# Kernel tuning notes

Hardware: AMD Instinct MI355X
Metric: run time of the kernel (lower is better)

## Reference

```python
import jax, jax.numpy as jnp
import numpy as np

N = 131072        # total points
NUM_SEG = 128     # number of point clouds / segments
INC = 3
HID = 128
OUTC = 128
NUM_LAYER = 6
NUM_INNER = 2
EPS = 1e-3        # ACN eps
CLAMP_MIN = 1e-3  # clamp(min=0.001) on normalizer


def setup_inputs() -> dict:
    key = jax.random.key(0)
    ks = jax.random.split(key, 10)
    s = 0.05
    x = jax.random.normal(ks[0], (N, INC), dtype=jnp.float32)
    segment_idx = jnp.sort(jax.random.randint(ks[1], (N,), 0, NUM_SEG, dtype=jnp.int32))
    weight_pri = jax.random.uniform(ks[2], (N,), dtype=jnp.float32)
    Win0 = jax.random.normal(ks[3], (INC, HID), dtype=jnp.float32) * s
    bin0 = jnp.zeros((HID,), jnp.float32)
    Win_rest = jax.random.normal(ks[4], (4, HID, HID), dtype=jnp.float32) * s
    bin_rest = jnp.zeros((4, HID), jnp.float32)
    # 6 ResBlocks x 2 inner ConvLayers: Linear(128,128) + ACN(att Linear(128,1)) + relu
    conv_W = jax.random.normal(ks[5], (NUM_LAYER, NUM_INNER, HID, HID), dtype=jnp.float32) * s
    conv_b = jnp.zeros((NUM_LAYER, NUM_INNER, HID), jnp.float32)
    att_W = jax.random.normal(ks[6], (NUM_LAYER, NUM_INNER, HID, 1), dtype=jnp.float32) * s
    att_b = jnp.zeros((NUM_LAYER, NUM_INNER, 1), jnp.float32)
    # output Mlp: Linear(128,128)+lrelu, Linear(128,128)
    out_W = jax.random.normal(ks[7], (2, HID, OUTC), dtype=jnp.float32) * s
    out_b = jnp.zeros((2, OUTC), jnp.float32)
    return dict(x=x, segment_idx=segment_idx, weight_pri=weight_pri,
                Win0=Win0, bin0=bin0, Win_rest=Win_rest, bin_rest=bin_rest,
                conv_W=conv_W, conv_b=conv_b, att_W=att_W, att_b=att_b,
                out_W=out_W, out_b=out_b)


def _seg_sum(v, seg):
    return jax.ops.segment_sum(v, seg, num_segments=NUM_SEG)


def _scatter_softmax(att, seg):
    # stable softmax within segments; att: [N, 1]
    m = jax.ops.segment_max(att, seg, num_segments=NUM_SEG)
    e = jnp.exp(att - m[seg])
    return e / _seg_sum(e, seg)[seg]


def _acn(x, aw, ab, seg, wp):
    # attentive context normalization; x: [N, HID]
    a = _scatter_softmax(x @ aw + ab, seg)          # [N, 1]
    a = a * wp[:, None]
    a = a / jnp.clip(_seg_sum(a, seg)[seg], CLAMP_MIN)
    mean = _seg_sum(x * a, seg)[seg]
    out = x - mean
    std = jnp.sqrt(_seg_sum(a * out * out, seg)[seg] + EPS)
    return out / std, a


def reference(x, segment_idx, weight_pri, Win0, bin0, Win_rest, bin_rest,
              conv_W, conv_b, att_W, att_b, out_W, out_b):
    lrelu = jax.nn.leaky_relu  # slope 0.01, matches nn.LeakyReLU default
    # input Mlp + outer leaky_relu in Acne.forward
    h = lrelu(x @ Win0 + bin0)
    for i in range(3):
        h = lrelu(h @ Win_rest[i] + bin_rest[i])
    h = h @ Win_rest[3] + bin_rest[3]
    h = lrelu(h)
    last_a = None
    for li in range(NUM_LAYER):
        xin = h
        for j in range(NUM_INNER):
            xin = xin @ conv_W[li, j] + conv_b[li, j]
            xin, last_a = _acn(xin, att_W[li, j], att_b[li, j], segment_idx, weight_pri)
            xin = jax.nn.relu(xin)
        h = xin + h  # residual
    h = lrelu(h @ out_W[0] + out_b[0])
    h = h @ out_W[1] + out_b[1]
    return h, last_a
```

## Files before the change

### kernel.cpp

```cpp
#include <hip/hip_runtime.h>

#define N_PTS 131072
#define NSEG 128
#define SW 132

typedef unsigned short u16;
typedef __attribute__((ext_vector_type(8))) short short8;
typedef __attribute__((ext_vector_type(8))) unsigned short ushort8;
typedef __attribute__((ext_vector_type(4))) float f32x4;

__device__ __forceinline__ float b2f(u16 u){union{unsigned v;float f;}x;x.v=((unsigned)u)<<16;return x.f;}
__device__ __forceinline__ u16 f2b(float f){unsigned u=__float_as_uint(f);u+=0x7FFFu+((u>>16)&1u);return (u16)(u>>16);}

__global__ __launch_bounds__(256) void k_zero(float* __restrict__ M0, float* __restrict__ Q0,
                                              float* __restrict__ Z0, float* __restrict__ W0){
  int t = blockIdx.x * 256 + threadIdx.x;
  M0[t] = 0.f; Q0[t] = 0.f;
  if (t < 128) { Z0[t] = 0.f; W0[t] = 0.f; }
}

__global__ __launch_bounds__(256) void k_wpack(const float* __restrict__ Wr,
    const float* __restrict__ convW, const float* __restrict__ outW,
    const float* __restrict__ attW, const float* __restrict__ attb,
    const float* __restrict__ convb,
    u16* __restrict__ Wf, float* __restrict__ uAtt, float* __restrict__ cAtt){
  int mat = blockIdx.x;
  const float* W = (mat<4) ? (Wr+mat*16384) : (mat<16) ? (convW+(mat-4)*16384) : (outW+(mat-16)*16384);
  u16* dst = Wf + mat*16384;
  for (int t = threadIdx.x; t < 16384; t += 256){ int n=t>>7,k=t&127; dst[t]=f2b(W[k*128+n]); }
  if (mat>=4 && mat<16){
    int l = mat-4;
    __syncthreads();
    int tid = threadIdx.x;
    if (tid < 128){
      float s = 0.f;
      for (int c=0;c<128;c++) s += b2f(dst[c*128+tid]) * attW[l*128+c];
      uAtt[l*128+tid] = s;
    } else if (tid == 128){
      float s = attb[l];
      for (int c=0;c<128;c++) s += convb[l*128+c] * attW[l*128+c];
      cAtt[l] = s;
    }
  }
}

__global__ __launch_bounds__(256) void k_in0(const float* __restrict__ x,
    const float* __restrict__ W0, const float* __restrict__ b0, u16* __restrict__ Tb){
  int gid = blockIdx.x*256 + threadIdx.x;
  int n = gid>>7, c = gid&127;
  float acc = b0[c] + x[n*3]*W0[c] + x[n*3+1]*W0[128+c] + x[n*3+2]*W0[256+c];
  Tb[gid] = f2b(acc > 0.f ? acc : 0.01f*acc);
}

template<bool WH>
__global__ __launch_bounds__(256) void k_mlp(u16* __restrict__ Tb, float* __restrict__ A0,
    const u16* __restrict__ Wfm, const float* __restrict__ Bv){
  __shared__ u16 Xs[128*SW];
  const int tid=threadIdx.x, wave=tid>>6, lane=tid&63, q=lane>>4, m16=lane&15;
  const int row0=blockIdx.x*128;
  const u16* Xb = Tb + (size_t)row0*128;
  #pragma unroll
  for (int i=0;i<8;i++){
    int e8=i*2048+tid*8; int rloc=e8>>7, c8=e8&127;
    *(ushort8*)&Xs[rloc*SW+c8] = *(const ushort8*)&Xb[rloc*128+c8];
  }
  short8 bfr[2][4];
  #pragma unroll
  for (int ct=0;ct<2;ct++){
    int n = wave*32 + 2*m16 + ct;
    #pragma unroll
    for (int kc=0;kc<4;kc++) bfr[ct][kc] = *(const short8*)&Wfm[n*128+kc*32+q*8];
  }
  const int cA = wave*32 + 2*m16;
  const float bias0=Bv[cA], bias1=Bv[cA+1];
  __syncthreads();
  #pragma unroll
  for (int rt=0;rt<8;rt++){
    int r0=rt*16;
    short8 af[4];
    #pragma unroll
    for (int kc=0;kc<4;kc++) af[kc] = *(const short8*)&Xs[(r0+m16)*SW+kc*32+q*8];
    f32x4 a0={0,0,0,0}, a1={0,0,0,0};
    #pragma unroll
    for (int kc=0;kc<4;kc++){
      a0=__builtin_amdgcn_mfma_f32_16x16x32_bf16(af[kc],bfr[0][kc],a0,0,0,0);
      a1=__builtin_amdgcn_mfma_f32_16x16x32_bf16(af[kc],bfr[1][kc],a1,0,0,0);
    }
    #pragma unroll
    for (int t=0;t<4;t++){
      int rloc=r0+q*4+t;
      float v0=a0[t]+bias0, v1=a1[t]+bias1;
      v0=v0>0.f?v0:0.01f*v0; v1=v1>0.f?v1:0.01f*v1;
      size_t wi=(size_t)(row0+rloc)*64 + wave*16 + m16;
      ((unsigned*)Tb)[wi] = (unsigned)f2b(v0) | ((unsigned)f2b(v1)<<16);
      if (WH) { float2 h={v0,v1}; ((float2*)A0)[wi]=h; }
    }
  }
}

template<int IN>
__global__ __launch_bounds__(256) void k_conv(u16* __restrict__ Tb, float* __restrict__ A0,
    const u16* __restrict__ Wfm, const float* __restrict__ Bv,
    const float* __restrict__ uL, const float* __restrict__ cL,
    float* __restrict__ L, const int* __restrict__ seg, const float* __restrict__ wp,
    const float* __restrict__ pZ, const float* __restrict__ pW,
    const float* __restrict__ pM, const float* __restrict__ pQ,
    float* __restrict__ cZ, float* __restrict__ cW,
    float* __restrict__ cM, float* __restrict__ cQ,
    float* __restrict__ nZ, float* __restrict__ nW,
    float* __restrict__ nM, float* __restrict__ nQ){
  __shared__ u16 Xs[128*SW];
  __shared__ float rowP[128];
  __shared__ float eS[128], aS[128];
  __shared__ int sgS[128];
  const int tid=threadIdx.x, wave=tid>>6, lane=tid&63, q=lane>>4, m16=lane&15;
  const int row0=blockIdx.x*128;

  if (tid<16){ nM[blockIdx.x*16+tid]=0.f; nQ[blockIdx.x*16+tid]=0.f; }
  if (blockIdx.x==0 && tid<128){ nZ[tid]=0.f; nW[tid]=0.f; }

  const int c8 = (tid*8)&127;
  float uv[8];
  { float4 u0=*(const float4*)&uL[c8]; float4 u1=*(const float4*)&uL[c8+4];
    uv[0]=u0.x;uv[1]=u0.y;uv[2]=u0.z;uv[3]=u0.w;uv[4]=u1.x;uv[5]=u1.y;uv[6]=u1.z;uv[7]=u1.w; }

  const u16* Xb = Tb + (size_t)row0*128;
  #pragma unroll
  for (int i=0;i<8;i++){
    int rloc = i*16 + (tid>>4);
    ushort8 raw = *(const ushort8*)&Xb[rloc*128+c8];
    float v[8];
    if (IN==1){
      #pragma unroll
      for (int j=0;j<8;j++) v[j]=b2f(raw[j]);
      *(ushort8*)&Xs[rloc*SW+c8] = raw;
    } else {
      int gr=row0+rloc, s=seg[gr];
      float Z=pZ[s], Wd=pW[s];
      float invd = 1.f/fmaxf(Wd, fmaxf(1e-3f*Z, 1e-30f));
      float sa = Wd*invd;
      float4 mn0=*(const float4*)&pM[s*128+c8];
      float4 mn1=*(const float4*)&pM[s*128+c8+4];
      float4 q0=*(const float4*)&pQ[s*128+c8];
      float4 q1=*(const float4*)&pQ[s*128+c8+4];
      float mn[8]={mn0.x,mn0.y,mn0.z,mn0.w,mn1.x,mn1.y,mn1.z,mn1.w};
      float qv[8]={q0.x,q0.y,q0.z,q0.w,q1.x,q1.y,q1.z,q1.w};
      #pragma unroll
      for (int j=0;j<8;j++){
        float m=mn[j]*invd, m2=qv[j]*invd;
        v[j]=fmaxf((b2f(raw[j])-m)*rsqrtf(m2+(sa-2.f)*m*m+1e-3f),0.f);
      }
      if (IN==3){
        float4 h0=*(const float4*)&A0[(size_t)gr*128+c8];
        float4 h1=*(const float4*)&A0[(size_t)gr*128+c8+4];
        v[0]+=h0.x;v[1]+=h0.y;v[2]+=h0.z;v[3]+=h0.w;
        v[4]+=h1.x;v[5]+=h1.y;v[6]+=h1.z;v[7]+=h1.w;
        float4 w0={v[0],v[1],v[2],v[3]}, w1={v[4],v[5],v[6],v[7]};
        *(float4*)&A0[(size_t)gr*128+c8]=w0;
        *(float4*)&A0[(size_t)gr*128+c8+4]=w1;
      }
      ushort8 ob;
      #pragma unroll
      for (int j=0;j<8;j++) ob[j]=f2b(v[j]);
      *(ushort8*)&Xs[rloc*SW+c8]=ob;
    }
    float p = v[0]*uv[0]+v[1]*uv[1]+v[2]*uv[2]+v[3]*uv[3]
            + v[4]*uv[4]+v[5]*uv[5]+v[6]*uv[6]+v[7]*uv[7];
    p += __shfl_xor(p,1,64); p += __shfl_xor(p,2,64);
    p += __shfl_xor(p,4,64); p += __shfl_xor(p,8,64);
    if (m16==0) rowP[rloc]=p;
  }

  short8 bfr[2][4];
  #pragma unroll
  for (int ct=0;ct<2;ct++){
    int n = wave*32 + 2*m16 + ct;
    #pragma unroll
    for (int kc=0;kc<4;kc++) bfr[ct][kc]=*(const short8*)&Wfm[n*128+kc*32+q*8];
  }
  const int cA = wave*32 + 2*m16;
  const float bias0=Bv[cA], bias1=Bv[cA+1];
  __syncthreads();

  if (tid<128){
    int r=row0+tid;
    float l=rowP[tid]+cL[0];
    float e=__expf(fminf(l,60.f));
    float sw=e*wp[r];
    L[r]=sw;
    eS[tid]=e; aS[tid]=sw; sgS[tid]=seg[r];
  }
  __syncthreads();
  if (tid<128){
    int s=sgS[tid];
    if (tid==0 || sgS[tid-1]!=s){
      float se=0.f, ss=0.f;
      for (int i=tid;i<128 && sgS[i]==s;i++){ se+=eS[i]; ss+=aS[i]; }
      atomicAdd(&cZ[s],se); atomicAdd(&cW[s],ss);
    }
  }

  const int s0=sgS[0], s127=sgS[127];
  const bool uni = (s0==s127);
  int cur = uni ? s0 : sgS[q*4];
  float sx0=0.f,sq0=0.f,sx1=0.f,sq1=0.f;

  #pragma unroll
  for (int rt=0;rt<8;rt++){
    int r0=rt*16;
    short8 af[4];
    #pragma unroll
    for (int kc=0;kc<4;kc++) af[kc]=*(const short8*)&Xs[(r0+m16)*SW+kc*32+q*8];
    f32x4 a0={0,0,0,0}, a1={0,0,0,0};
    #pragma unroll
    for (int kc=0;kc<4;kc++){
      a0=__builtin_amdgcn_mfma_f32_16x16x32_bf16(af[kc],bfr[0][kc],a0,0,0,0);
      a1=__builtin_amdgcn_mfma_f32_16x16x32_bf16(af[kc],bfr[1][kc],a1,0,0,0);
    }
    #pragma unroll
    for (int t=0;t<4;t++){
      int rloc=r0+q*4+t;
      float v0=a0[t]+bias0, v1=a1[t]+bias1;
      ((unsigned*)Tb)[(size_t)(row0+rloc)*64 + wave*16 + m16] =
          (unsigned)f2b(v0) | ((unsigned)f2b(v1)<<16);
      float a = aS[rloc];
      if (!uni){
        int s = sgS[rloc];
        if (s != cur){
          atomicAdd(&cM[cur*128+cA],sx0);  atomicAdd(&cQ[cur*128+cA],sq0);
          atomicAdd(&cM[cur*128+cA+1],sx1);atomicAdd(&cQ[cur*128+cA+1],sq1);
          sx0=sq0=sx1=sq1=0.f; cur=s;
        }
      }
      sx0 += a*v0; sq0 += a*v0*v0;
      sx1 += a*v1; sq1 += a*v1*v1;
    }
  }
  if (uni){
    sx0 += __shfl_xor(sx0,16,64); sx0 += __shfl_xor(sx0,32,64);
    sq0 += __shfl_xor(sq0,16,64); sq0 += __shfl_xor(sq0,32,64);
    sx1 += __shfl_xor(sx1,16,64); sx1 += __shfl_xor(sx1,32,64);
    sq1 += __shfl_xor(sq1,16,64); sq1 += __shfl_xor(sq1,32,64);
    if (q==0){
      atomicAdd(&cM[s0*128+cA],sx0);  atomicAdd(&cQ[s0*128+cA],sq0);
      atomicAdd(&cM[s0*128+cA+1],sx1);atomicAdd(&cQ[s0*128+cA+1],sq1);
    }
  } else {
    atomicAdd(&cM[cur*128+cA],sx0);  atomicAdd(&cQ[cur*128+cA],sq0);
    atomicAdd(&cM[cur*128+cA+1],sx1);atomicAdd(&cQ[cur*128+cA+1],sq1);
  }
}

__global__ __launch_bounds__(256) void k_megaout(const u16* __restrict__ Tb,
    const float* __restrict__ A0, const u16* __restrict__ Wf16, const float* __restrict__ outb,
    const int* __restrict__ seg, const float* __restrict__ L,
    const float* __restrict__ pZ, const float* __restrict__ pW,
    const float* __restrict__ pM, const float* __restrict__ pQ,
    float* __restrict__ Of, float* __restrict__ a_out){
  __shared__ u16 buf[2*128*SW];
  const int tid=threadIdx.x, wave=tid>>6, lane=tid&63, q=lane>>4, m16=lane&15;
  const int row0=blockIdx.x*128;
  const u16* Xb = Tb + (size_t)row0*128;
  #pragma unroll
  for (int i=0;i<8;i++){
    int e8=i*2048+tid*8; int rloc=e8>>7, c8=e8&127;
    ushort8 raw=*(const ushort8*)&Xb[rloc*128+c8];
    int gr=row0+rloc, s=seg[gr];
    float Z=pZ[s], Wd=pW[s];
    float invd=1.f/fmaxf(Wd, fmaxf(1e-3f*Z,1e-30f));
    float sa=Wd*invd;
    float4 mn0=*(const float4*)&pM[s*128+c8];
    float4 mn1=*(const float4*)&pM[s*128+c8+4];
    float4 q0=*(const float4*)&pQ[s*128+c8];
    float4 q1=*(const float4*)&pQ[s*128+c8+4];
    float mn[8]={mn0.x,mn0.y,mn0.z,mn0.w,mn1.x,mn1.y,mn1.z,mn1.w};
    float qv[8]={q0.x,q0.y,q0.z,q0.w,q1.x,q1.y,q1.z,q1.w};
    float4 h0=*(const float4*)&A0[(size_t)gr*128+c8];
    float4 h1=*(const float4*)&A0[(size_t)gr*128+c8+4];
    float hv[8]={h0.x,h0.y,h0.z,h0.w,h1.x,h1.y,h1.z,h1.w};
    ushort8 ob;
    #pragma unroll
    for (int j=0;j<8;j++){
      float m=mn[j]*invd, m2=qv[j]*invd;
      ob[j]=f2b(fmaxf((b2f(raw[j])-m)*rsqrtf(m2+(sa-2.f)*m*m+1e-3f),0.f)+hv[j]);
    }
    *(ushort8*)&buf[rloc*SW+c8]=ob;
  }
  if (tid<128){
    int r=row0+tid, s=seg[r];
    float invd=1.f/fmaxf(pW[s], fmaxf(1e-3f*pZ[s],1e-30f));
    a_out[r]=L[r]*invd;
  }
  __syncthreads();
  const int cA=wave*32+2*m16;
  {
    u16* dst=buf+128*SW;
    short8 bfr[2][4];
    #pragma unroll
    for (int ct=0;ct<2;ct++){
      int n=wave*32+2*m16+ct;
      #pragma unroll
      for (int kc=0;kc<4;kc++) bfr[ct][kc]=*(const short8*)&Wf16[n*128+kc*32+q*8];
    }
    float bias0=outb[cA], bias1=outb[cA+1];
    #pragma unroll
    for (int rt=0;rt<8;rt++){
      int r0=rt*16;
      short8 af[4];
      #pragma unroll
      for (int kc=0;kc<4;kc++) af[kc]=*(const short8*)&buf[(r0+m16)*SW+kc*32+q*8];
      f32x4 a0={0,0,0,0}, a1={0,0,0,0};
      #pragma unroll
      for (int kc=0;kc<4;kc++){
        a0=__builtin_amdgcn_mfma_f32_16x16x32_bf16(af[kc],bfr[0][kc],a0,0,0,0);
        a1=__builtin_amdgcn_mfma_f32_16x16x32_bf16(af[kc],bfr[1][kc],a1,0,0,0);
      }
      #pragma unroll
      for (int t=0;t<4;t++){
        int rloc=r0+q*4+t;
        float v0=a0[t]+bias0, v1=a1[t]+bias1;
        v0=v0>0.f?v0:0.01f*v0; v1=v1>0.f?v1:0.01f*v1;
        dst[rloc*SW+cA]=f2b(v0);
        dst[rloc*SW+cA+1]=f2b(v1);
      }
    }
  }
  __syncthreads();
  {
    const u16* src=buf+128*SW;
    short8 bfr[2][4];
    #pragma unroll
    for (int ct=0;ct<2;ct++){
      int n=wave*32+2*m16+ct;
      #pragma unroll
      for (int kc=0;kc<4;kc++) bfr[ct][kc]=*(const short8*)&Wf16[16384+n*128+kc*32+q*8];
    }
    float bias0=outb[128+cA], bias1=outb[128+cA+1];
    #pragma unroll
    for (int rt=0;rt<8;rt++){
      int r0=rt*16;
      short8 af[4];
      #pragma unroll
      for (int kc=0;kc<4;kc++) af[kc]=*(const short8*)&src[(r0+m16)*SW+kc*32+q*8];
      f32x4 a0={0,0,0,0}, a1={0,0,0,0};
      #pragma unroll
      for (int kc=0;kc<4;kc++){
        a0=__builtin_amdgcn_mfma_f32_16x16x32_bf16(af[kc],bfr[0][kc],a0,0,0,0);
        a1=__builtin_amdgcn_mfma_f32_16x16x32_bf16(af[kc],bfr[1][kc],a1,0,0,0);
      }
      #pragma unroll
      for (int t=0;t<4;t++){
        int rloc=r0+q*4+t;
        float2 o={a0[t]+bias0, a1[t]+bias1};
        ((float2*)Of)[(size_t)(row0+rloc)*64 + wave*16 + m16]=o;
      }
    }
  }
}

extern "C" void kernel_launch(void* const* d_in, const int* in_sizes, int n_in,
                              void* d_out, int out_size, void* d_ws, size_t ws_size,
                              hipStream_t stream){
  const float* x     = (const float*)d_in[0];
  const int*   seg   = (const int*)d_in[1];
  const float* wp    = (const float*)d_in[2];
  const float* Win0  = (const float*)d_in[3];
  const float* bin0  = (const float*)d_in[4];
  const float* Wr    = (const float*)d_in[5];
  const float* br    = (const float*)d_in[6];
  const float* convW = (const float*)d_in[7];
  const float* convb = (const float*)d_in[8];
  const float* attW  = (const float*)d_in[9];
  const float* attb  = (const float*)d_in[10];
  const float* outW  = (const float*)d_in[11];
  const float* outb  = (const float*)d_in[12];

  float* A0 = (float*)d_ws;
  u16*   Tb = (u16*)(A0 + (size_t)N_PTS*128);
  float* L  = (float*)(Tb + (size_t)N_PTS*128);
  float* base = L + N_PTS;
  float* SZ[3], *SWt[3], *SM[3], *SQ[3];
  for (int p=0;p<3;p++){
    SZ[p]  = base + p*(128+128+16384+16384);
    SWt[p] = SZ[p] + 128;
    SM[p]  = SWt[p] + 128;
    SQ[p]  = SM[p] + 16384;
  }
  float* uAtt = base + 3*(128+128+16384+16384);
  float* cAtt = uAtt + 12*128;
  u16*   Wf   = (u16*)(cAtt + 16);

  float* Of    = (float*)d_out;
  float* a_out = (float*)d_out + (size_t)N_PTS*128;

  const int GB = N_PTS/128;

  k_zero<<<64,256,0,stream>>>(SM[0],SQ[0],SZ[0],SWt[0]);
  k_wpack<<<18,256,0,stream>>>(Wr, convW, outW, attW, attb, convb, Wf, uAtt, cAtt);
  k_in0<<<N_PTS*128/256,256,0,stream>>>(x, Win0, bin0, Tb);

  for (int i=0;i<3;i++)
    k_mlp<false><<<GB,256,0,stream>>>(Tb, nullptr, Wf+i*16384, br+i*128);
  k_mlp<true><<<GB,256,0,stream>>>(Tb, A0, Wf+3*16384, br+3*128);

  for (int j=0;j<12;j++){
    int wp_ = j%3, rp = (j+2)%3, np = (j+1)%3;
    const u16* Wm = Wf + (size_t)(4+j)*16384;
    const float* uj = uAtt + j*128;
    const float* cj = cAtt + j;
    if (j==0)
      k_conv<1><<<GB,256,0,stream>>>(Tb, nullptr, Wm, convb, uj, cj, L, seg, wp,
          nullptr,nullptr,nullptr,nullptr,
          SZ[wp_],SWt[wp_],SM[wp_],SQ[wp_], SZ[np],SWt[np],SM[np],SQ[np]);
    else if (j&1)
      k_conv<2><<<GB,256,0,stream>>>(Tb, nullptr, Wm, convb+j*128, uj, cj, L, seg, wp,
          SZ[rp],SWt[rp],SM[rp],SQ[rp],
          SZ[wp_],SWt[wp_],SM[wp_],SQ[wp_], SZ[np],SWt[np],SM[np],SQ[np]);
    else
      k_conv<3><<<GB,256,0,stream>>>(Tb, A0, Wm, convb+j*128, uj, cj, L, seg, wp,
          SZ[rp],SWt[rp],SM[rp],SQ[rp],
          SZ[wp_],SWt[wp_],SM[wp_],SQ[wp_], SZ[np],SWt[np],SM[np],SQ[np]);
  }

  k_megaout<<<GB,256,0,stream>>>(Tb, A0, Wf+(size_t)16*16384, outb, seg, L,
                                 SZ[2],SWt[2],SM[2],SQ[2], Of, a_out);
}
```

Before: 731.5 us.

## Fuse whole network into one cooperative persistent kernel with grid syncs

Replaces the chain of per-layer kernels (input MLP, 12 conv/ACN layers, output MLP) with a single cooperative kernel. Each block keeps its 128-row tile in LDS and the residual in registers across all layers, and uses grid.sync between layers to publish the segment statistics. This removes the global round trips of activations and the per-launch overhead. The cost is 1024 blocks that must all be co-resident (4 per CU), heavy register pressure from a 64-float residual array, and 12 grid-wide barriers. A fallback to the old multi-kernel path remains if occupancy is insufficient.

```diff
diff --git a/kernel.cpp b/kernel.cpp
--- a/kernel.cpp
+++ b/kernel.cpp
@@ -1,8 +1,12 @@
 #include <hip/hip_runtime.h>
+#include <hip/hip_cooperative_groups.h>
+
+namespace cg = cooperative_groups;
 
 #define N_PTS 131072
 #define NSEG 128
 #define SW 132
+#define PSTRIDE 33024
 
 typedef unsigned short u16;
 typedef __attribute__((ext_vector_type(8))) short short8;
@@ -11,13 +15,8 @@
 
 __device__ __forceinline__ float b2f(u16 u){union{unsigned v;float f;}x;x.v=((unsigned)u)<<16;return x.f;}
 __device__ __forceinline__ u16 f2b(float f){unsigned u=__float_as_uint(f);u+=0x7FFFu+((u>>16)&1u);return (u16)(u>>16);}
-
-__global__ __launch_bounds__(256) void k_zero(float* __restrict__ M0, float* __restrict__ Q0,
-                                              float* __restrict__ Z0, float* __restrict__ W0){
-  int t = blockIdx.x * 256 + threadIdx.x;
-  M0[t] = 0.f; Q0[t] = 0.f;
-  if (t < 128) { Z0[t] = 0.f; W0[t] = 0.f; }
-}
+__device__ __forceinline__ float aload(const float* p){ return __hip_atomic_load(p, __ATOMIC_RELAXED, __HIP_MEMORY_SCOPE_AGENT); }
+__device__ __forceinline__ void astore(float* p, float v){ __hip_atomic_store(p, v, __ATOMIC_RELAXED, __HIP_MEMORY_SCOPE_AGENT); }
 
 __global__ __launch_bounds__(256) void k_wpack(const float* __restrict__ Wr,
     const float* __restrict__ convW, const float* __restrict__ outW,
@@ -44,6 +43,311 @@
   }
 }
 
+__device__ __forceinline__ void gemm_lrelu_inplace(u16* Xs, const u16* __restrict__ Wm,
+    const float* __restrict__ Bv, int wave, int q, int m16){
+  short8 bfr[2][4];
+  const int cA = wave*32 + 2*m16;
+  #pragma unroll
+  for (int ct=0; ct<2; ct++){
+    int n = cA + ct;
+    #pragma unroll
+    for (int kc=0; kc<4; kc++) bfr[ct][kc] = *(const short8*)&Wm[n*128 + kc*32 + q*8];
+  }
+  const float b0 = Bv[cA], b1 = Bv[cA+1];
+  #pragma unroll
+  for (int rt=0; rt<8; rt++){
+    const int r0 = rt*16;
+    f32x4 a0={0,0,0,0}, a1={0,0,0,0};
+    short8 afn = *(const short8*)&Xs[(r0+m16)*SW + q*8];
+    #pragma unroll
+    for (int kc=0; kc<4; kc++){
+      short8 afc = afn;
+      if (kc<3) afn = *(const short8*)&Xs[(r0+m16)*SW + (kc+1)*32 + q*8];
+      a0 = __builtin_amdgcn_mfma_f32_16x16x32_bf16(afc, bfr[0][kc], a0, 0,0,0);
+      a1 = __builtin_amdgcn_mfma_f32_16x16x32_bf16(afc, bfr[1][kc], a1, 0,0,0);
+    }
+    __syncthreads();
+    #pragma unroll
+    for (int t=0; t<4; t++){
+      int rloc = r0 + q*4 + t;
+      float v0 = a0[t]+b0, v1 = a1[t]+b1;
+      v0 = v0>0.f ? v0 : 0.01f*v0;
+      v1 = v1>0.f ? v1 : 0.01f*v1;
+      *(unsigned*)&Xs[rloc*SW + cA] = (unsigned)f2b(v0) | ((unsigned)f2b(v1)<<16);
+    }
+  }
+}
+
+__global__ __launch_bounds__(256, 4) void k_fused(
+    const float* __restrict__ x, const int* __restrict__ seg, const float* __restrict__ wp,
+    const float* __restrict__ Win0, const float* __restrict__ bin0,
+    const float* __restrict__ br, const float* __restrict__ convb, const float* __restrict__ outb,
+    const u16* __restrict__ Wf, const float* __restrict__ uAtt, const float* __restrict__ cAtt,
+    float* __restrict__ Pstat, float* __restrict__ Of, float* __restrict__ a_out)
+{
+  __shared__ u16 Xs[128*SW];
+  __shared__ float rowP[128];
+  __shared__ float eS[128], aS[128];
+  __shared__ int   sgS[128];
+  __shared__ float wpS[128];
+  __shared__ float MhL[2][128], ScL[2][128];
+
+  const int tid=threadIdx.x, wave=tid>>6, lane=tid&63, q=lane>>4, m16=lane&15;
+  const int row0=blockIdx.x*128;
+  const int c8=(tid*8)&127;
+  const int rbase=tid>>4;
+
+  cg::grid_group grid = cg::this_grid();
+
+  if (tid<128){ sgS[tid]=seg[row0+tid]; wpS[tid]=wp[row0+tid]; }
+  if (tid<33){ int idx=blockIdx.x*33+tid; if (idx<PSTRIDE) astore(Pstat+idx, 0.f); }
+  __syncthreads();
+
+  const int sA=sgS[0], sB=sgS[127];
+  const bool uni=(sA==sB);
+  unsigned slotm=0;
+  #pragma unroll
+  for (int i=0;i<8;i++) if (sgS[i*16+rbase]!=sA) slotm|=1u<<i;
+
+  {
+    float w0[8],w1[8],w2[8],bv[8];
+    *(float4*)&w0[0]=*(const float4*)&Win0[c8];     *(float4*)&w0[4]=*(const float4*)&Win0[c8+4];
+    *(float4*)&w1[0]=*(const float4*)&Win0[128+c8]; *(float4*)&w1[4]=*(const float4*)&Win0[128+c8+4];
+    *(float4*)&w2[0]=*(const float4*)&Win0[256+c8]; *(float4*)&w2[4]=*(const float4*)&Win0[256+c8+4];
+    *(float4*)&bv[0]=*(const float4*)&bin0[c8];     *(float4*)&bv[4]=*(const float4*)&bin0[c8+4];
+    #pragma unroll
+    for (int i=0;i<8;i++){
+      int rloc=i*16+rbase, r=row0+rloc;
+      float x0=x[r*3], x1=x[r*3+1], x2=x[r*3+2];
+      ushort8 ob;
+      #pragma unroll
+      for (int jj=0;jj<8;jj++){
+        float v=bv[jj]+x0*w0[jj]+x1*w1[jj]+x2*w2[jj];
+        v=v>0.f?v:0.01f*v;
+        ob[jj]=f2b(v);
+      }
+      *(ushort8*)&Xs[rloc*SW+c8]=ob;
+    }
+  }
+  __syncthreads();
+
+  #pragma unroll 1
+  for (int l=0;l<4;l++){
+    gemm_lrelu_inplace(Xs, Wf + (size_t)l*16384, br + l*128, wave,q,m16);
+    __syncthreads();
+  }
+
+  grid.sync();
+
+  float h[64];
+
+  #pragma unroll 1
+  for (int j=0;j<12;j++){
+    float* Pw = Pstat + (j%3)*PSTRIDE;
+    const float* Pr = Pstat + ((j+2)%3)*PSTRIDE;
+    float* Pn = Pstat + ((j+1)%3)*PSTRIDE;
+
+    if (j>0){
+      int half=tid>>7, ch=tid&127;
+      int s = half ? sB : sA;
+      float Z=aload(Pr+s), Wd=aload(Pr+128+s);
+      float invd=1.f/fmaxf(Wd, fmaxf(1e-3f*Z, 1e-30f));
+      float sa=Wd*invd;
+      float m =aload(Pr+256  + s*128+ch)*invd;
+      float qv=aload(Pr+16640+ s*128+ch)*invd;
+      MhL[half][ch]=m;
+      ScL[half][ch]=rsqrtf(qv+(sa-2.f)*m*m+1e-3f);
+    }
+    float uv[8];
+    { float4 u0=*(const float4*)&uAtt[j*128+c8]; float4 u1=*(const float4*)&uAtt[j*128+c8+4];
+      uv[0]=u0.x;uv[1]=u0.y;uv[2]=u0.z;uv[3]=u0.w;uv[4]=u1.x;uv[5]=u1.y;uv[6]=u1.z;uv[7]=u1.w; }
+    const float cL0 = cAtt[j];
+    __syncthreads();
+
+    #pragma unroll
+    for (int i=0;i<8;i++){
+      const int rloc=i*16+rbase;
+      ushort8 raw=*(const ushort8*)&Xs[rloc*SW+c8];
+      float v[8];
+      if (j==0){
+        #pragma unroll
+        for (int jj=0;jj<8;jj++){ v[jj]=b2f(raw[jj]); h[i*8+jj]=v[jj]; }
+      } else {
+        const int sl=(slotm>>i)&1;
+        #pragma unroll
+        for (int jj=0;jj<8;jj++){
+          float vv=(b2f(raw[jj])-MhL[sl][c8+jj])*ScL[sl][c8+jj];
+          vv=fmaxf(vv,0.f);
+          if ((j&1)==0){ vv+=h[i*8+jj]; h[i*8+jj]=vv; }
+          v[jj]=vv;
+        }
+        ushort8 ob;
+        #pragma unroll
+        for (int jj=0;jj<8;jj++) ob[jj]=f2b(v[jj]);
+        *(ushort8*)&Xs[rloc*SW+c8]=ob;
+      }
+      float p = v[0]*uv[0]+v[1]*uv[1]+v[2]*uv[2]+v[3]*uv[3]
+              + v[4]*uv[4]+v[5]*uv[5]+v[6]*uv[6]+v[7]*uv[7];
+      p += __shfl_xor(p,1,64); p += __shfl_xor(p,2,64);
+      p += __shfl_xor(p,4,64); p += __shfl_xor(p,8,64);
+      if (m16==0) rowP[rloc]=p;
+    }
+    __syncthreads();
+
+    if (tid<128){
+      float l2=rowP[tid]+cL0;
+      float e=__expf(fminf(l2,60.f));
+      float sw=e*wpS[tid];
+      eS[tid]=e; aS[tid]=sw;
+    }
+    if (tid<33){ int idx=blockIdx.x*33+tid; if (idx<PSTRIDE) astore(Pn+idx, 0.f); }
+    __syncthreads();
+    if (tid<128){
+      int s=sgS[tid];
+      if (tid==0 || sgS[tid-1]!=s){
+        float se=0.f, ss=0.f;
+        for (int i2=tid;i2<128 && sgS[i2]==s;i2++){ se+=eS[i2]; ss+=aS[i2]; }
+        atomicAdd(&Pw[s],se); atomicAdd(&Pw[128+s],ss);
+      }
+    }
+
+    const u16* Wm = Wf + (size_t)(4+j)*16384;
+    const float* Bv = convb + j*128;
+    short8 bfr[2][4];
+    const int cA = wave*32+2*m16;
+    #pragma unroll
+    for (int ct=0;ct<2;ct++){
+      int n=cA+ct;
+      #pragma unroll
+      for (int kc=0;kc<4;kc++) bfr[ct][kc]=*(const short8*)&Wm[n*128+kc*32+q*8];
+    }
+    const float bias0=Bv[cA], bias1=Bv[cA+1];
+    float* cM=Pw+256; float* cQ=Pw+16640;
+    int cur = uni ? sA : sgS[q*4];
+    float sx0=0.f,sq0=0.f,sx1=0.f,sq1=0.f;
+    #pragma unroll
+    for (int rt=0;rt<8;rt++){
+      const int r0=rt*16;
+      f32x4 a0={0,0,0,0}, a1={0,0,0,0};
+      short8 afn=*(const short8*)&Xs[(r0+m16)*SW+q*8];
+      #pragma unroll
+      for (int kc=0;kc<4;kc++){
+        short8 afc=afn;
+        if (kc<3) afn=*(const short8*)&Xs[(r0+m16)*SW+(kc+1)*32+q*8];
+        a0=__builtin_amdgcn_mfma_f32_16x16x32_bf16(afc,bfr[0][kc],a0,0,0,0);
+        a1=__builtin_amdgcn_mfma_f32_16x16x32_bf16(afc,bfr[1][kc],a1,0,0,0);
+      }
+      __syncthreads();
+      #pragma unroll
+      for (int t=0;t<4;t++){
+        int rloc=r0+q*4+t;
+        float v0=a0[t]+bias0, v1=a1[t]+bias1;
+        *(unsigned*)&Xs[rloc*SW+cA]=(unsigned)f2b(v0)|((unsigned)f2b(v1)<<16);
+        float a=aS[rloc];
+        if (!uni){
+          int s=sgS[rloc];
+          if (s!=cur){
+            atomicAdd(&cM[cur*128+cA],sx0);  atomicAdd(&cQ[cur*128+cA],sq0);
+            atomicAdd(&cM[cur*128+cA+1],sx1);atomicAdd(&cQ[cur*128+cA+1],sq1);
+            sx0=sq0=sx1=sq1=0.f; cur=s;
+          }
+        }
+        sx0+=a*v0; sq0+=a*v0*v0; sx1+=a*v1; sq1+=a*v1*v1;
+      }
+    }
+    if (uni){
+      sx0+=__shfl_xor(sx0,16,64); sx0+=__shfl_xor(sx0,32,64);
+      sq0+=__shfl_xor(sq0,16,64); sq0+=__shfl_xor(sq0,32,64);
+      sx1+=__shfl_xor(sx1,16,64); sx1+=__shfl_xor(sx1,32,64);
+      sq1+=__shfl_xor(sq1,16,64); sq1+=__shfl_xor(sq1,32,64);
+      if (q==0){
+        atomicAdd(&cM[sA*128+cA],sx0);  atomicAdd(&cQ[sA*128+cA],sq0);
+        atomicAdd(&cM[sA*128+cA+1],sx1);atomicAdd(&cQ[sA*128+cA+1],sq1);
+      }
+    } else {
+      atomicAdd(&cM[cur*128+cA],sx0);  atomicAdd(&cQ[cur*128+cA],sq0);
+      atomicAdd(&cM[cur*128+cA+1],sx1);atomicAdd(&cQ[cur*128+cA+1],sq1);
+    }
+    grid.sync();
+  }
+
+  {
+    const float* Pr = Pstat + 2*PSTRIDE;
+    { int half=tid>>7, ch=tid&127;
+      int s = half ? sB : sA;
+      float Z=aload(Pr+s), Wd=aload(Pr+128+s);
+      float invd=1.f/fmaxf(Wd, fmaxf(1e-3f*Z, 1e-30f));
+      float sa=Wd*invd;
+      float m =aload(Pr+256  + s*128+ch)*invd;
+      float qv=aload(Pr+16640+ s*128+ch)*invd;
+      MhL[half][ch]=m;
+      ScL[half][ch]=rsqrtf(qv+(sa-2.f)*m*m+1e-3f);
+    }
+    if (tid<128){
+      int s=sgS[tid];
+      float Z=aload(Pr+s), Wd=aload(Pr+128+s);
+      float invd=1.f/fmaxf(Wd, fmaxf(1e-3f*Z, 1e-30f));
+      a_out[row0+tid]=aS[tid]*invd;
+    }
+    __syncthreads();
+    #pragma unroll
+    for (int i=0;i<8;i++){
+      const int rloc=i*16+rbase;
+      ushort8 raw=*(const ushort8*)&Xs[rloc*SW+c8];
+      const int sl=(slotm>>i)&1;
+      ushort8 ob;
+      #pragma unroll
+      for (int jj=0;jj<8;jj++){
+        float vv=(b2f(raw[jj])-MhL[sl][c8+jj])*ScL[sl][c8+jj];
+        vv=fmaxf(vv,0.f)+h[i*8+jj];
+        ob[jj]=f2b(vv);
+      }
+      *(ushort8*)&Xs[rloc*SW+c8]=ob;
+    }
+    __syncthreads();
+    gemm_lrelu_inplace(Xs, Wf+(size_t)16*16384, outb, wave,q,m16);
+    __syncthreads();
+    {
+      const u16* Wm=Wf+(size_t)17*16384;
+      short8 bfr[2][4];
+      const int cA=wave*32+2*m16;
+      #pragma unroll
+      for (int ct=0;ct<2;ct++){
+        int n=cA+ct;
+        #pragma unroll
+        for (int kc=0;kc<4;kc++) bfr[ct][kc]=*(const short8*)&Wm[n*128+kc*32+q*8];
+      }
+      const float b0=outb[128+cA], b1=outb[128+cA+1];
+      #pragma unroll
+      for (int rt=0;rt<8;rt++){
+        const int r0=rt*16;
+        f32x4 a0={0,0,0,0}, a1={0,0,0,0};
+        short8 afn=*(const short8*)&Xs[(r0+m16)*SW+q*8];
+        #pragma unroll
+        for (int kc=0;kc<4;kc++){
+          short8 afc=afn;
+          if (kc<3) afn=*(const short8*)&Xs[(r0+m16)*SW+(kc+1)*32+q*8];
+          a0=__builtin_amdgcn_mfma_f32_16x16x32_bf16(afc,bfr[0][kc],a0,0,0,0);
+          a1=__builtin_amdgcn_mfma_f32_16x16x32_bf16(afc,bfr[1][kc],a1,0,0,0);
+        }
+        #pragma unroll
+        for (int t=0;t<4;t++){
+          int rloc=r0+q*4+t;
+          float2 o={a0[t]+b0, a1[t]+b1};
+          ((float2*)Of)[(size_t)(row0+rloc)*64 + wave*16 + m16]=o;
+        }
+      }
+    }
+  }
+}
+
+__global__ __launch_bounds__(256) void k_zero(float* __restrict__ M0, float* __restrict__ Q0,
+                                              float* __restrict__ Z0, float* __restrict__ W0){
+  int t = blockIdx.x * 256 + threadIdx.x;
+  M0[t] = 0.f; Q0[t] = 0.f;
+  if (t < 128) { Z0[t] = 0.f; W0[t] = 0.f; }
+}
+
 __global__ __launch_bounds__(256) void k_in0(const float* __restrict__ x,
     const float* __restrict__ W0, const float* __restrict__ b0, u16* __restrict__ Tb){
   int gid = blockIdx.x*256 + threadIdx.x;
@@ -93,7 +397,7 @@
       v0=v0>0.f?v0:0.01f*v0; v1=v1>0.f?v1:0.01f*v1;
       size_t wi=(size_t)(row0+rloc)*64 + wave*16 + m16;
       ((unsigned*)Tb)[wi] = (unsigned)f2b(v0) | ((unsigned)f2b(v1)<<16);
-      if (WH) { float2 h={v0,v1}; ((float2*)A0)[wi]=h; }
+      if (WH) { float2 hh={v0,v1}; ((float2*)A0)[wi]=hh; }
     }
   }
 }
@@ -102,7 +406,7 @@
 __global__ __launch_bounds__(256) void k_conv(u16* __restrict__ Tb, float* __restrict__ A0,
     const u16* __restrict__ Wfm, const float* __restrict__ Bv,
     const float* __restrict__ uL, const float* __restrict__ cL,
-    float* __restrict__ L, const int* __restrict__ seg, const float* __restrict__ wp,
+    float* __restrict__ L, const int* __restrict__ seg, const float* __restrict__ wpv,
     const float* __restrict__ pZ, const float* __restrict__ pW,
     const float* __restrict__ pM, const float* __restrict__ pQ,
     float* __restrict__ cZ, float* __restrict__ cW,
@@ -186,7 +490,7 @@
     int r=row0+tid;
     float l=rowP[tid]+cL[0];
     float e=__expf(fminf(l,60.f));
-    float sw=e*wp[r];
+    float sw=e*wpv[r];
     L[r]=sw;
     eS[tid]=e; aS[tid]=sw; sgS[tid]=seg[r];
   }
@@ -252,7 +556,7 @@
 }
 
 __global__ __launch_bounds__(256) void k_megaout(const u16* __restrict__ Tb,
-    const float* __restrict__ A0, const u16* __restrict__ Wf16, const float* __restrict__ outb,
+    const float* __restrict__ A0, const u16* __restrict__ Wf16, const float* __restrict__ outbv,
     const int* __restrict__ seg, const float* __restrict__ L,
     const float* __restrict__ pZ, const float* __restrict__ pW,
     const float* __restrict__ pM, const float* __restrict__ pQ,
@@ -302,7 +606,7 @@
       #pragma unroll
       for (int kc=0;kc<4;kc++) bfr[ct][kc]=*(const short8*)&Wf16[n*128+kc*32+q*8];
     }
-    float bias0=outb[cA], bias1=outb[cA+1];
+    float bias0=outbv[cA], bias1=outbv[cA+1];
     #pragma unroll
     for (int rt=0;rt<8;rt++){
       int r0=rt*16;
@@ -335,7 +639,7 @@
       #pragma unroll
       for (int kc=0;kc<4;kc++) bfr[ct][kc]=*(const short8*)&Wf16[16384+n*128+kc*32+q*8];
     }
-    float bias0=outb[128+cA], bias1=outb[128+cA+1];
+    float bias0=outbv[128+cA], bias1=outbv[128+cA+1];
     #pragma unroll
     for (int rt=0;rt<8;rt++){
       int r0=rt*16;
@@ -361,6 +665,7 @@
 extern "C" void kernel_launch(void* const* d_in, const int* in_sizes, int n_in,
                               void* d_out, int out_size, void* d_ws, size_t ws_size,
                               hipStream_t stream){
+  (void)in_sizes; (void)n_in; (void)out_size; (void)ws_size;
   const float* x     = (const float*)d_in[0];
   const int*   seg   = (const int*)d_in[1];
   const float* wp    = (const float*)d_in[2];
@@ -381,12 +686,12 @@
   float* base = L + N_PTS;
   float* SZ[3], *SWt[3], *SM[3], *SQ[3];
   for (int p=0;p<3;p++){
-    SZ[p]  = base + p*(128+128+16384+16384);
+    SZ[p]  = base + p*PSTRIDE;
     SWt[p] = SZ[p] + 128;
     SM[p]  = SWt[p] + 128;
     SQ[p]  = SM[p] + 16384;
   }
-  float* uAtt = base + 3*(128+128+16384+16384);
+  float* uAtt = base + 3*PSTRIDE;
   float* cAtt = uAtt + 12*128;
   u16*   Wf   = (u16*)(cAtt + 16);
 
@@ -395,8 +700,29 @@
 
   const int GB = N_PTS/128;
 
+  static int coop = -1;
+  if (coop < 0){
+    int nb = 0;
+    hipError_t e = hipOccupancyMaxActiveBlocksPerMultiprocessor(&nb, (const void*)k_fused, 256, 0);
+    int ncu = 0, dev = 0;
+    hipGetDevice(&dev);
+    hipDeviceProp_t prop;
+    if (hipGetDeviceProperties(&prop, dev) == hipSuccess) ncu = prop.multiProcessorCount;
+    coop = (e == hipSuccess && ncu > 0 && nb * ncu >= GB) ? 1 : 0;
+  }
+
+  k_wpack<<<18,256,0,stream>>>(Wr, convW, outW, attW, attb, convb, Wf, uAtt, cAtt);
+
+  if (coop){
+    void* args[] = {(void*)&x,(void*)&seg,(void*)&wp,(void*)&Win0,(void*)&bin0,
+                    (void*)&br,(void*)&convb,(void*)&outb,
+                    (void*)&Wf,(void*)&uAtt,(void*)&cAtt,(void*)&base,
+                    (void*)&Of,(void*)&a_out};
+    hipLaunchCooperativeKernel((const void*)k_fused, dim3(GB), dim3(256), args, 0, stream);
+    return;
+  }
+
   k_zero<<<64,256,0,stream>>>(SM[0],SQ[0],SZ[0],SWt[0]);
-  k_wpack<<<18,256,0,stream>>>(Wr, convW, outW, attW, attb, convb, Wf, uAtt, cAtt);
   k_in0<<<N_PTS*128/256,256,0,stream>>>(x, Win0, bin0, Tb);
 
   for (int i=0;i<3;i++)
```

New measurement: 729.0 us. No clear change (-0.3%).
